# Optimization experiments

Measured on AMD Instinct MI355X. Metric: run time of the kernel, lower is better.

## Reference

```python
import jax, jax.numpy as jnp
import numpy as np

EMBED_DIM = 1024
NUM_HEADS = 16
HEAD_DIM = EMBED_DIM // NUM_HEADS
WINDOW = 3
N_RAND = 3
BLOCK = 64
BATCH = 2
SEQ = 2048


def _bigbird_mask(seq_len: int) -> np.ndarray:
    """Global + sliding-window + random block mask. True = attend.
    Deterministic (fixed numpy seed) stand-in for np.random.choice in the
    original; the mask is data-independent so it is a compile-time constant."""
    nb = -(-seq_len // BLOCK)  # ceil division
    mask = np.zeros((seq_len, seq_len), dtype=bool)
    g = min(BLOCK, seq_len)
    mask[:g, :] = True  # global rows
    mask[:, :g] = True  # global cols
    blk = np.arange(seq_len) // BLOCK
    # sliding window: block distance <= WINDOW (matches start/end block loop)
    mask |= np.abs(blk[:, None] - blk[None, :]) <= WINDOW
    rng = np.random.RandomState(0)
    for b in range(1, nb):
        avail = [x for x in range(1, nb) if abs(x - b) > WINDOW]
        if avail:
            sel = rng.choice(avail, size=min(N_RAND, len(avail)), replace=False)
            s0, s1 = b * BLOCK, min(seq_len, (b + 1) * BLOCK)
            for rb in sel:
                mask[s0:s1, rb * BLOCK:min(seq_len, (rb + 1) * BLOCK)] = True
    return mask


def setup_inputs() -> dict:
    key = jax.random.key(0)
    ks = jax.random.split(key, 9)
    E = EMBED_DIM
    std = E ** -0.5
    return {
        "hidden_states": jax.random.normal(ks[0], (BATCH, SEQ, E), jnp.float32),
        "wq": jax.random.normal(ks[1], (E, E), jnp.float32) * std,
        "bq": jnp.zeros((E,), jnp.float32),
        "wk": jax.random.normal(ks[2], (E, E), jnp.float32) * std,
        "bk": jnp.zeros((E,), jnp.float32),
        "wv": jax.random.normal(ks[3], (E, E), jnp.float32) * std,
        "bv": jnp.zeros((E,), jnp.float32),
        "wo": jax.random.normal(ks[4], (E, E), jnp.float32) * std,
        "bo": jnp.zeros((E,), jnp.float32),
    }


def reference(hidden_states, wq, bq, wk, bk, wv, bv, wo, bo):
    B, S, E = hidden_states.shape
    D = HEAD_DIM
    scale = D ** -0.5

    def proj(w, b):  # (B,S,E) -> (B,H,S,D)
        return (hidden_states @ w.T + b).reshape(B, S, NUM_HEADS, D).transpose(0, 2, 1, 3)

    q = proj(wq, bq)
    k = proj(wk, bk)
    v = proj(wv, bv)
    scores = jnp.einsum('bhqd,bhkd->bhqk', q, k) * scale  # dense, masked post-hoc (as in source)
    mask = jnp.asarray(_bigbird_mask(S))
    scores = jnp.where(mask[None, None, :, :], scores, -jnp.inf)
    attn = jax.nn.softmax(scores, axis=-1)
    out = jnp.einsum('bhqk,bhkd->bhqd', attn, v)
    out = out.transpose(0, 2, 1, 3).reshape(B, S, E)
    return out @ wo.T + bo
```

## Files before the change

### kernel.cpp

```cpp
#include <hip/hip_runtime.h>
#include <cstdint>
#include <math.h>


#define DEVI __device__ __forceinline__

typedef __bf16 bf16x8 __attribute__((ext_vector_type(8)));
typedef float floatx4 __attribute__((ext_vector_type(4)));
typedef unsigned short u16x8 __attribute__((ext_vector_type(8)));
typedef unsigned short u16x4 __attribute__((ext_vector_type(4)));
typedef unsigned short ushort_t;

typedef const __attribute__((address_space(1))) void* gptr_as1;
typedef __attribute__((address_space(3))) void* lptr_as3;

DEVI ushort_t f2bf(float f) {
  unsigned u = __float_as_uint(f);
  unsigned r = ((u >> 16) & 1u) + 0x7fffu;
  return (ushort_t)((u + r) >> 16);
}

DEVI void lds_load16(void* lds, const void* g) {
  __builtin_amdgcn_global_load_lds((gptr_as1)g, (lptr_as3)lds, 16, 0, 0);
}

DEVI floatx4 mfma16(bf16x8 a, bf16x8 b, floatx4 c) {
  return __builtin_amdgcn_mfma_f32_16x16x32_bf16(a, b, c, 0, 0, 0);
}

#define BARR() do { asm volatile("" ::: "memory"); \
                    __builtin_amdgcn_s_barrier();  \
                    asm volatile("" ::: "memory"); } while (0)
#define VMC(N) asm volatile("s_waitcnt vmcnt(" #N ")" ::: "memory")

struct MTState { unsigned mt[624]; int mti; };

constexpr unsigned mt_next(MTState& s) {
  if (s.mti >= 624) {
    for (int k = 0; k < 624; ++k) {
      unsigned y = (s.mt[k] & 0x80000000u) | (s.mt[(k + 1) % 624] & 0x7fffffffu);
      unsigned v = s.mt[(k + 397) % 624] ^ (y >> 1);
      if (y & 1u) v ^= 0x9908b0dfu;
      s.mt[k] = v;
    }
    s.mti = 0;
  }
  unsigned y = s.mt[s.mti++];
  y ^= y >> 11;
  y ^= (y << 7) & 0x9d2c5680u;
  y ^= (y << 15) & 0xefc60000u;
  y ^= y >> 18;
  return y;
}

constexpr unsigned mt_interval(MTState& s, unsigned mx) {
  if (mx == 0u) return 0u;
  unsigned msk = mx;
  msk |= msk >> 1; msk |= msk >> 2; msk |= msk >> 4; msk |= msk >> 8; msk |= msk >> 16;
  unsigned v = mt_next(s) & msk;
  while (v > mx) v = mt_next(s) & msk;
  return v;
}

struct MaskPack { unsigned char list[32][32]; int cnt[32]; };

constexpr MaskPack make_pack() {
  unsigned char m[32][32] = {};
  for (int i = 0; i < 32; ++i)
    for (int j = 0; j < 32; ++j) {
      int d = i - j; if (d < 0) d = -d;
      m[i][j] = (i == 0 || j == 0 || d <= 3) ? (unsigned char)1 : (unsigned char)0;
    }
  MTState st{};
  st.mt[0] = 0u;
  for (int i = 1; i < 624; ++i)
    st.mt[i] = 1812433253u * (st.mt[i - 1] ^ (st.mt[i - 1] >> 30)) + (unsigned)i;
  st.mti = 624;
  for (int b = 1; b < 32; ++b) {
    int avail[32] = {}; int n = 0;
    for (int x = 1; x < 32; ++x) {
      int d = x - b; if (d < 0) d = -d;
      if (d > 3) avail[n++] = x;
    }
    if (n == 0) continue;
    int perm[32] = {};
    for (int i = 0; i < n; ++i) perm[i] = i;
    for (int i = n - 1; i > 0; --i) {
      unsigned j = mt_interval(st, (unsigned)i);
      int t = perm[i]; perm[i] = perm[(int)j]; perm[(int)j] = t;
    }
    int take = n < 3 ? n : 3;
    for (int s = 0; s < take; ++s) m[b][avail[perm[s]]] = 1;
  }
  MaskPack P{};
  for (int i = 0; i < 32; ++i) {
    int c = 0;
    for (int j = 0; j < 32; ++j)
      if (m[i][j]) P.list[i][c++] = (unsigned char)j;
    P.cnt[i] = c;
  }
  return P;
}

__constant__ MaskPack MP = make_pack();

__global__ __launch_bounds__(256) void cvt_all(
    const float* __restrict__ hs, const float* __restrict__ wq,
    const float* __restrict__ wk, const float* __restrict__ wv,
    const float* __restrict__ wo,
    ushort_t* __restrict__ hs_bf, ushort_t* __restrict__ wq_bf,
    ushort_t* __restrict__ wk_bf, ushort_t* __restrict__ wv_bf,
    ushort_t* __restrict__ wo_bf) {
  const int i = blockIdx.x * 256 + threadIdx.x;
  const float* s;
  ushort_t* d;
  int j;
  if (i < 1048576) {
    s = hs; d = hs_bf; j = i;
  } else {
    const int t = (i - 1048576) >> 18;
    j = (i - 1048576) & 262143;
    s = t == 0 ? wq : (t == 1 ? wk : (t == 2 ? wv : wo));
    d = t == 0 ? wq_bf : (t == 1 ? wk_bf : (t == 2 ? wv_bf : wo_bf));
  }
  const float4 f = ((const float4*)s)[j];
  u16x4 o;
  o.x = f2bf(f.x); o.y = f2bf(f.y); o.z = f2bf(f.z); o.w = f2bf(f.w);
  ((u16x4*)d)[j] = o;
}

DEVI void stage_half(ushort_t* ldsb, const ushort_t* g, int w, int l) {
  lds_load16(ldsb + w * 1024 + l * 8, g);
  lds_load16(ldsb + w * 1024 + 512 + l * 8, g + 8192);
}

DEVI void rdA(bf16x8 (&a)[4][2], const ushort_t* base, int wm, int li, int quad) {
#pragma unroll
  for (int mi = 0; mi < 4; ++mi) {
    const int rh = wm * 64 + mi * 16 + li;
    const int sw = rh & 7;
#pragma unroll
    for (int ks = 0; ks < 2; ++ks)
      a[mi][ks] = *(const bf16x8*)(base + rh * 64 + (((ks * 4 + quad) ^ sw) << 3));
  }
}

DEVI void rdB(bf16x8 (&b)[2][2], const ushort_t* base, int wn, int li, int quad) {
#pragma unroll
  for (int ni = 0; ni < 2; ++ni) {
    const int rh = wn * 32 + ni * 16 + li;
    const int sw = rh & 7;
#pragma unroll
    for (int ks = 0; ks < 2; ++ks)
      b[ni][ks] = *(const bf16x8*)(base + rh * 64 + (((ks * 4 + quad) ^ sw) << 3));
  }
}

DEVI void mm16(floatx4 (&c)[4][2], const bf16x8 (&a)[4][2], const bf16x8 (&b)[2][2]) {
  __builtin_amdgcn_s_setprio(1);
#pragma unroll
  for (int ks = 0; ks < 2; ++ks)
#pragma unroll
    for (int mi = 0; mi < 4; ++mi)
#pragma unroll
      for (int ni = 0; ni < 2; ++ni)
        c[mi][ni] = mfma16(a[mi][ks], b[ni][ks], c[mi][ni]);
  __builtin_amdgcn_s_setprio(0);
}

__global__ __launch_bounds__(512, 2) void gemm_qkv_fused(
    const ushort_t* __restrict__ A,
    const ushort_t* __restrict__ W0, const ushort_t* __restrict__ W1,
    const ushort_t* __restrict__ W2,
    const float* __restrict__ bq, const float* __restrict__ bk,
    const float* __restrict__ bv,
    ushort_t* __restrict__ Qo, ushort_t* __restrict__ Ko,
    ushort_t* __restrict__ Vt) {
  __shared__ alignas(16) ushort_t LDS[2][2][2][8192];
  const int tid = threadIdx.x;
  const int w = tid >> 6, l = tid & 63, quad = l >> 4, li = l & 15;
  const int wm = w >> 2, wn = w & 3;
  const int bid = blockIdx.x;
  const int swz = (bid & 7) * 24 + (bid >> 3);
  const int m0 = (swz / 12) << 8;
  const int n0g = (swz % 12) << 8;
  const int z = n0g >> 10, n0l = n0g & 1023;
  const ushort_t* Bw = z == 0 ? W0 : (z == 1 ? W1 : W2);
  const float* bias = z == 0 ? bq : (z == 1 ? bk : bv);

  const int rst = w * 16 + (l >> 3);
  const int cst = ((l & 7) ^ (l >> 3)) << 3;
  const ushort_t* gA = A + (size_t)(m0 + rst) * 1024 + cst;
  const ushort_t* gB = Bw + (size_t)(n0l + rst) * 1024 + cst;

  const floatx4 fz = {0.0f, 0.0f, 0.0f, 0.0f};
  floatx4 acc[2][2][4][2];
#pragma unroll
  for (int qm = 0; qm < 2; ++qm)
#pragma unroll
    for (int qn = 0; qn < 2; ++qn)
#pragma unroll
      for (int mi = 0; mi < 4; ++mi)
#pragma unroll
        for (int ni = 0; ni < 2; ++ni) acc[qm][qn][mi][ni] = fz;

  bf16x8 a[4][2], b0[2][2], b1[2][2];

  stage_half(&LDS[0][0][0][0], gA, w, l);
  stage_half(&LDS[0][0][1][0], gA + 131072, w, l);
  stage_half(&LDS[0][1][0][0], gB, w, l);
  stage_half(&LDS[0][1][1][0], gB + 131072, w, l);
  stage_half(&LDS[1][0][0][0], gA + 64, w, l);
  stage_half(&LDS[1][1][0][0], gB + 64, w, l);
  stage_half(&LDS[1][1][1][0], gB + 131072 + 64, w, l);
  VMC(6);
  BARR();

#pragma unroll 1
  for (int it = 0; it < 8; ++it) {
    const bool pf = (it < 7);
    const int o_cy = (2 * it + 1) * 64;
    const int o_x = (2 * it + 2) * 64;
    const int o_y = (2 * it + 3) * 64;

    rdA(a, &LDS[0][0][0][0], wm, li, quad);
    rdB(b0, &LDS[0][1][0][0], wn, li, quad);
    stage_half(&LDS[1][0][1][0], gA + 131072 + o_cy, w, l);
    mm16(acc[0][0], a, b0);
    BARR();

    rdB(b1, &LDS[0][1][1][0], wn, li, quad);
    if (pf) stage_half(&LDS[0][0][0][0], gA + o_x, w, l);
    mm16(acc[0][1], a, b1);
    BARR();

    rdA(a, &LDS[0][0][1][0], wm, li, quad);
    if (pf) stage_half(&LDS[0][1][0][0], gB + o_x, w, l);
    mm16(acc[1][0], a, b0);
    BARR();

    if (pf) stage_half(&LDS[0][1][1][0], gB + 131072 + o_x, w, l);
    mm16(acc[1][1], a, b1);
    if (pf) { VMC(6); } else { VMC(0); }
    BARR();

    rdA(a, &LDS[1][0][0][0], wm, li, quad);
    rdB(b0, &LDS[1][1][0][0], wn, li, quad);
    if (pf) stage_half(&LDS[0][0][1][0], gA + 131072 + o_x, w, l);
    mm16(acc[0][0], a, b0);
    BARR();

    rdB(b1, &LDS[1][1][1][0], wn, li, quad);
    if (pf) stage_half(&LDS[1][0][0][0], gA + o_y, w, l);
    mm16(acc[0][1], a, b1);
    BARR();

    rdA(a, &LDS[1][0][1][0], wm, li, quad);
    if (pf) stage_half(&LDS[1][1][0][0], gB + o_y, w, l);
    mm16(acc[1][0], a, b0);
    BARR();

    if (pf) stage_half(&LDS[1][1][1][0], gB + 131072 + o_y, w, l);
    mm16(acc[1][1], a, b1);
    if (pf) { VMC(6); }
    BARR();
  }

  const float qs = (z == 0) ? 0.18033688011112042f : 1.0f;
#pragma unroll
  for (int Qm = 0; Qm < 2; ++Qm)
#pragma unroll
    for (int Qn = 0; Qn < 2; ++Qn)
#pragma unroll
      for (int ni = 0; ni < 2; ++ni) {
        const int col = n0l + Qn * 128 + wn * 32 + ni * 16 + li;
        const float bb_ = bias[col];
        if (z == 2) {
          const int hh = col >> 6, dd = col & 63;
#pragma unroll
          for (int mi = 0; mi < 4; ++mi) {
            const int row0 = m0 + Qm * 128 + wm * 64 + mi * 16 + quad * 4;
            const int bb = row0 >> 11, s0 = row0 & 2047;
            u16x4 pk;
#pragma unroll
            for (int r = 0; r < 4; ++r) pk[r] = f2bf(acc[Qm][Qn][mi][ni][r] + bb_);
            *(u16x4*)(Vt + (size_t)((bb * 16 + hh) * 64 + dd) * 2048 + s0) = pk;
          }
        } else {
          ushort_t* Co = (z == 0) ? Qo : Ko;
#pragma unroll
          for (int mi = 0; mi < 4; ++mi)
#pragma unroll
            for (int r = 0; r < 4; ++r) {
              const int row = m0 + Qm * 128 + wm * 64 + mi * 16 + quad * 4 + r;
              Co[(size_t)row * 1024 + col] = f2bf((acc[Qm][Qn][mi][ni][r] + bb_) * qs);
            }
        }
      }
}

__global__ __launch_bounds__(256) void gemm_o64(
    const ushort_t* __restrict__ A, const ushort_t* __restrict__ W,
    const float* __restrict__ bias, float* __restrict__ C) {
  constexpr int N = 1024, K = 1024;
  __shared__ alignas(16) ushort_t As[64 * 32];
  __shared__ alignas(16) ushort_t Bs[128 * 32];
  const int tid = threadIdx.x;
  const int w = tid >> 6, l = tid & 63, quad = l >> 4, li = l & 15;
  const int m0 = blockIdx.x * 64, n0 = blockIdx.y * 128;
  const int wm = (w >> 1) * 32, wn = (w & 1) * 64;

  const int lofA = w * 512 + l * 8;
  const int rA = lofA >> 5, cA = lofA & 31;
  const int lofB0 = (w * 2 + 0) * 512 + l * 8;
  const int lofB1 = (w * 2 + 1) * 512 + l * 8;
  const int rB0 = lofB0 >> 5, cB0 = lofB0 & 31;
  const int rB1 = lofB1 >> 5, cB1 = lofB1 & 31;
  const ushort_t* gA = A + (size_t)(m0 + rA) * K + cA;
  const ushort_t* gB0 = W + (size_t)(n0 + rB0) * K + cB0;
  const ushort_t* gB1 = W + (size_t)(n0 + rB1) * K + cB1;

  const floatx4 fzero = {0.0f, 0.0f, 0.0f, 0.0f};
  floatx4 acc[2][4];
#pragma unroll
  for (int i = 0; i < 2; ++i)
#pragma unroll
    for (int j = 0; j < 4; ++j) acc[i][j] = fzero;

  for (int k0 = 0; k0 < K; k0 += 32) {
    lds_load16(As + lofA, gA + k0);
    lds_load16(Bs + lofB0, gB0 + k0);
    lds_load16(Bs + lofB1, gB1 + k0);
    __syncthreads();
    bf16x8 af[2], bfr[4];
#pragma unroll
    for (int mi = 0; mi < 2; ++mi)
      af[mi] = *(const bf16x8*)(As + (wm + mi * 16 + li) * 32 + quad * 8);
#pragma unroll
    for (int ni = 0; ni < 4; ++ni)
      bfr[ni] = *(const bf16x8*)(Bs + (wn + ni * 16 + li) * 32 + quad * 8);
#pragma unroll
    for (int mi = 0; mi < 2; ++mi)
#pragma unroll
      for (int ni = 0; ni < 4; ++ni)
        acc[mi][ni] = mfma16(af[mi], bfr[ni], acc[mi][ni]);
    __syncthreads();
  }

#pragma unroll
  for (int ni = 0; ni < 4; ++ni) {
    const int col = n0 + wn + ni * 16 + li;
    const float bv = bias[col];
#pragma unroll
    for (int mi = 0; mi < 2; ++mi) {
#pragma unroll
      for (int r = 0; r < 4; ++r) {
        const int row = m0 + wm + mi * 16 + quad * 4 + r;
        C[(size_t)row * N + col] = acc[mi][ni][r] + bv;
      }
    }
  }
}

__global__ __launch_bounds__(256) void attn_kernel(
    const ushort_t* __restrict__ Q, const ushort_t* __restrict__ Kg,
    const ushort_t* __restrict__ Vtg, ushort_t* __restrict__ O,
    float* __restrict__ OP, float* __restrict__ LP) {
  __shared__ alignas(16) ushort_t Kls[64 * 72];
  __shared__ alignas(16) ushort_t Vls[64 * 72];
  __shared__ alignas(16) ushort_t Ps[4][16 * 76];

  const int tid = threadIdx.x;
  const int w = tid >> 6, l = tid & 63, quad = l >> 4, li = l & 15;
  const int hb = blockIdx.x;
  const int y = blockIdx.y;
  const bool partial = (y >= 31);
  const int qb = partial ? 0 : (y + 1);
  const int p = partial ? (y - 31) : 0;
  const int base = p * 11;
  const int nact = partial ? (32 - base < 11 ? 32 - base : 11) : MP.cnt[qb];

  const int h = hb & 15, b = hb >> 4;
  const size_t qoff = (size_t)b * 2048 * 1024 + (size_t)h * 64;
  const size_t vtoff = (size_t)hb * 64 * 2048;

  const int qrow = qb * 64 + w * 16 + li;
  const bf16x8 aq0 = *(const bf16x8*)(Q + qoff + (size_t)qrow * 1024 + quad * 8);
  const bf16x8 aq1 = *(const bf16x8*)(Q + qoff + (size_t)qrow * 1024 + 32 + quad * 8);

  const floatx4 fzero = {0.0f, 0.0f, 0.0f, 0.0f};
  floatx4 o_acc[4];
  float lp[4];
#pragma unroll
  for (int nt = 0; nt < 4; ++nt) o_acc[nt] = fzero;
#pragma unroll
  for (int r = 0; r < 4; ++r) lp[r] = 0.0f;

  const int r0 = w * 16 + (l >> 3);
  const int r1 = r0 + 8;
  const int cb = (l & 7) * 8;
  const ushort_t* kg0 = Kg + qoff + (size_t)r0 * 1024 + cb;
  const ushort_t* kg1 = Kg + qoff + (size_t)r1 * 1024 + cb;
  const ushort_t* vg0 = Vtg + vtoff + (size_t)r0 * 2048 + cb;
  const ushort_t* vg1 = Vtg + vtoff + (size_t)r1 * 2048 + cb;
  ushort_t* kd0 = Kls + r0 * 72 + cb;
  ushort_t* kd1 = Kls + r1 * 72 + cb;
  ushort_t* vd0 = Vls + r0 * 72 + cb;
  ushort_t* vd1 = Vls + r1 * 72 + cb;
  ushort_t* PsW = Ps[w];

  int kb = MP.list[qb][base];
  {
    const u16x8 a0 = *(const u16x8*)(kg0 + (size_t)kb * 65536);
    const u16x8 a1 = *(const u16x8*)(kg1 + (size_t)kb * 65536);
    const u16x8 b0 = *(const u16x8*)(vg0 + kb * 64);
    const u16x8 b1 = *(const u16x8*)(vg1 + kb * 64);
    *(u16x8*)kd0 = a0; *(u16x8*)kd1 = a1;
    *(u16x8*)vd0 = b0; *(u16x8*)vd1 = b1;
  }

  for (int i = 0; i < nact; ++i) {
    const bool pf = (i + 1 < nact);
    const int kbn = pf ? (int)MP.list[qb][base + i + 1] : 0;
    __syncthreads();

    u16x8 na0, na1, nb0, nb1;
    if (pf) {
      na0 = *(const u16x8*)(kg0 + (size_t)kbn * 65536);
      na1 = *(const u16x8*)(kg1 + (size_t)kbn * 65536);
      nb0 = *(const u16x8*)(vg0 + kbn * 64);
      nb1 = *(const u16x8*)(vg1 + kbn * 64);
    }

    floatx4 s[4];
#pragma unroll
    for (int nt = 0; nt < 4; ++nt) {
      const bf16x8 bk0 = *(const bf16x8*)(Kls + (nt * 16 + li) * 72 + quad * 8);
      const bf16x8 bk1 = *(const bf16x8*)(Kls + (nt * 16 + li) * 72 + 32 + quad * 8);
      s[nt] = mfma16(aq1, bk1, mfma16(aq0, bk0, fzero));
    }

#pragma unroll
    for (int nt = 0; nt < 4; ++nt)
#pragma unroll
      for (int r = 0; r < 4; ++r) {
        const float e = exp2f(s[nt][r]);
        lp[r] += e;
        PsW[(quad * 4 + r) * 76 + nt * 16 + li] = f2bf(e);
      }

#pragma unroll
    for (int c = 0; c < 2; ++c) {
      const bf16x8 pa = *(const bf16x8*)(PsW + li * 76 + c * 32 + quad * 8);
#pragma unroll
      for (int nt = 0; nt < 4; ++nt) {
        const bf16x8 vb = *(const bf16x8*)(Vls + (nt * 16 + li) * 72 + c * 32 + quad * 8);
        o_acc[nt] = mfma16(pa, vb, o_acc[nt]);
      }
    }

    __syncthreads();
    if (pf) {
      *(u16x8*)kd0 = na0; *(u16x8*)kd1 = na1;
      *(u16x8*)vd0 = nb0; *(u16x8*)vd1 = nb1;
    }
  }

#pragma unroll
  for (int stp = 1; stp <= 8; stp <<= 1)
#pragma unroll
    for (int r = 0; r < 4; ++r) lp[r] += __shfl_xor(lp[r], stp);

  if (!partial) {
#pragma unroll
    for (int r = 0; r < 4; ++r) {
      const float rinv = 1.0f / lp[r];
#pragma unroll
      for (int nt = 0; nt < 4; ++nt) {
        const float ov = o_acc[nt][r] * rinv;
        O[qoff + (size_t)(qb * 64 + w * 16 + quad * 4 + r) * 1024 + nt * 16 + li] = f2bf(ov);
      }
    }
  } else {
    float* O32 = OP + (size_t)(hb * 3 + p) * 4096;
    float* LPp = LP + (hb * 3 + p) * 64;
#pragma unroll
    for (int r = 0; r < 4; ++r) {
      const int row = w * 16 + quad * 4 + r;
#pragma unroll
      for (int nt = 0; nt < 4; ++nt)
        O32[row * 64 + nt * 16 + li] = o_acc[nt][r];
      if (li == 0) LPp[row] = lp[r];
    }
  }
}

__global__ __launch_bounds__(256) void combine_qb0(
    const float* __restrict__ OP, const float* __restrict__ LP,
    ushort_t* __restrict__ O) {
  const int hb = blockIdx.x;
  const int b = hb >> 4, h = hb & 15;
  const float* o0 = OP + (size_t)hb * 3 * 4096;
  const float* l0 = LP + hb * 3 * 64;
  for (int idx = threadIdx.x; idx < 4096; idx += 256) {
    const int q = idx >> 6, d = idx & 63;
    const float s = o0[idx] + o0[4096 + idx] + o0[8192 + idx];
    const float lsum = l0[q] + l0[64 + q] + l0[128 + q];
    O[(size_t)b * 2048 * 1024 + (size_t)q * 1024 + h * 64 + d] = f2bf(s / lsum);
  }
}

extern "C" void kernel_launch(void* const* d_in, const int* in_sizes, int n_in,
                              void* d_out, int out_size, void* d_ws, size_t ws_size,
                              hipStream_t stream) {
  const float* hs = (const float*)d_in[0];
  const float* wq = (const float*)d_in[1];
  const float* bq = (const float*)d_in[2];
  const float* wk = (const float*)d_in[3];
  const float* bk = (const float*)d_in[4];
  const float* wv = (const float*)d_in[5];
  const float* bv = (const float*)d_in[6];
  const float* wo = (const float*)d_in[7];
  const float* bo = (const float*)d_in[8];
  float* out = (float*)d_out;

  char* ws = (char*)d_ws;
  ushort_t* hs_bf = (ushort_t*)(ws);
  ushort_t* wq_bf = (ushort_t*)(ws + (8ull << 20));
  ushort_t* wk_bf = (ushort_t*)(ws + (10ull << 20));
  ushort_t* wv_bf = (ushort_t*)(ws + (12ull << 20));
  ushort_t* wo_bf = (ushort_t*)(ws + (14ull << 20));
  ushort_t* Qb = (ushort_t*)(ws + (16ull << 20));
  ushort_t* Kb = (ushort_t*)(ws + (24ull << 20));
  ushort_t* Vt = (ushort_t*)(ws + (32ull << 20));
  ushort_t* AO = hs_bf;
  float* OP = (float*)(ws + (10ull << 20));
  float* LP = (float*)((char*)OP + 32 * 3 * 4096 * sizeof(float));

  cvt_all<<<8192, 256, 0, stream>>>(hs, wq, wk, wv, wo,
                                    hs_bf, wq_bf, wk_bf, wv_bf, wo_bf);

  gemm_qkv_fused<<<192, 512, 0, stream>>>(hs_bf, wq_bf, wk_bf, wv_bf,
                                          bq, bk, bv, Qb, Kb, Vt);

  dim3 ga(32, 34, 1);
  attn_kernel<<<ga, 256, 0, stream>>>(Qb, Kb, Vt, AO, OP, LP);

  combine_qb0<<<32, 256, 0, stream>>>(OP, LP, AO);

  dim3 go(64, 8, 1);
  gemm_o64<<<go, 256, 0, stream>>>(AO, wo_bf, bo, out);
}
```

Measured before the change: 191.2 us.

## Process KV blocks in pairs with double-buffered K/V and P aliased into K LDS

```diff
diff --git a/kernel.cpp b/kernel.cpp
--- a/kernel.cpp
+++ b/kernel.cpp
@@ -366,9 +366,8 @@
     const ushort_t* __restrict__ Q, const ushort_t* __restrict__ Kg,
     const ushort_t* __restrict__ Vtg, ushort_t* __restrict__ O,
     float* __restrict__ OP, float* __restrict__ LP) {
-  __shared__ alignas(16) ushort_t Kls[64 * 72];
-  __shared__ alignas(16) ushort_t Vls[64 * 72];
-  __shared__ alignas(16) ushort_t Ps[4][16 * 76];
+  __shared__ alignas(16) ushort_t Kls[2][4608];
+  __shared__ alignas(16) ushort_t Vls[2][4608];
 
   const int tid = threadIdx.x;
   const int w = tid >> 6, l = tid & 63, quad = l >> 4, li = l & 15;
@@ -403,66 +402,139 @@
   const ushort_t* kg1 = Kg + qoff + (size_t)r1 * 1024 + cb;
   const ushort_t* vg0 = Vtg + vtoff + (size_t)r0 * 2048 + cb;
   const ushort_t* vg1 = Vtg + vtoff + (size_t)r1 * 2048 + cb;
-  ushort_t* kd0 = Kls + r0 * 72 + cb;
-  ushort_t* kd1 = Kls + r1 * 72 + cb;
-  ushort_t* vd0 = Vls + r0 * 72 + cb;
-  ushort_t* vd1 = Vls + r1 * 72 + cb;
-  ushort_t* PsW = Ps[w];
-
-  int kb = MP.list[qb][base];
+  const int sd0 = r0 * 72 + cb;
+  const int sd1 = r1 * 72 + cb;
+
+  ushort_t* Pall = &Kls[0][0];
+  ushort_t* PA = Pall + w * 1088;
+  ushort_t* PB = Pall + 4352 + w * 1088;
+
   {
-    const u16x8 a0 = *(const u16x8*)(kg0 + (size_t)kb * 65536);
-    const u16x8 a1 = *(const u16x8*)(kg1 + (size_t)kb * 65536);
-    const u16x8 b0 = *(const u16x8*)(vg0 + kb * 64);
-    const u16x8 b1 = *(const u16x8*)(vg1 + kb * 64);
-    *(u16x8*)kd0 = a0; *(u16x8*)kd1 = a1;
-    *(u16x8*)vd0 = b0; *(u16x8*)vd1 = b1;
-  }
-
-  for (int i = 0; i < nact; ++i) {
-    const bool pf = (i + 1 < nact);
-    const int kbn = pf ? (int)MP.list[qb][base + i + 1] : 0;
+    const int kb0 = MP.list[qb][base];
+    const u16x8 a0 = *(const u16x8*)(kg0 + (size_t)kb0 * 65536);
+    const u16x8 a1 = *(const u16x8*)(kg1 + (size_t)kb0 * 65536);
+    const u16x8 b0 = *(const u16x8*)(vg0 + kb0 * 64);
+    const u16x8 b1 = *(const u16x8*)(vg1 + kb0 * 64);
+    *(u16x8*)(&Kls[0][0] + sd0) = a0; *(u16x8*)(&Kls[0][0] + sd1) = a1;
+    *(u16x8*)(&Vls[0][0] + sd0) = b0; *(u16x8*)(&Vls[0][0] + sd1) = b1;
+    if (nact > 1) {
+      const int kb1 = MP.list[qb][base + 1];
+      const u16x8 c0 = *(const u16x8*)(kg0 + (size_t)kb1 * 65536);
+      const u16x8 c1 = *(const u16x8*)(kg1 + (size_t)kb1 * 65536);
+      const u16x8 d0 = *(const u16x8*)(vg0 + kb1 * 64);
+      const u16x8 d1 = *(const u16x8*)(vg1 + kb1 * 64);
+      *(u16x8*)(&Kls[1][0] + sd0) = c0; *(u16x8*)(&Kls[1][0] + sd1) = c1;
+      *(u16x8*)(&Vls[1][0] + sd0) = d0; *(u16x8*)(&Vls[1][0] + sd1) = d1;
+    }
+  }
+  __syncthreads();
+
+  const int npair = nact >> 1;
+#pragma unroll 1
+  for (int ip = 0; ip < npair; ++ip) {
+    const int i0 = 2 * ip;
+    const bool pfA = (i0 + 2 < nact);
+    const bool pfB = (i0 + 3 < nact);
+
+    u16x8 nkA0, nkA1, nvA0, nvA1, nkB0, nkB1, nvB0, nvB1;
+    if (pfA) {
+      const int kbn = MP.list[qb][base + i0 + 2];
+      nkA0 = *(const u16x8*)(kg0 + (size_t)kbn * 65536);
+      nkA1 = *(const u16x8*)(kg1 + (size_t)kbn * 65536);
+      nvA0 = *(const u16x8*)(vg0 + kbn * 64);
+      nvA1 = *(const u16x8*)(vg1 + kbn * 64);
+    }
+    if (pfB) {
+      const int kbn = MP.list[qb][base + i0 + 3];
+      nkB0 = *(const u16x8*)(kg0 + (size_t)kbn * 65536);
+      nkB1 = *(const u16x8*)(kg1 + (size_t)kbn * 65536);
+      nvB0 = *(const u16x8*)(vg0 + kbn * 64);
+      nvB1 = *(const u16x8*)(vg1 + kbn * 64);
+    }
+
+    floatx4 sA[4], sB[4];
+#pragma unroll
+    for (int nt = 0; nt < 4; ++nt) {
+      const bf16x8 k0 = *(const bf16x8*)(&Kls[0][0] + (nt * 16 + li) * 72 + quad * 8);
+      const bf16x8 k1 = *(const bf16x8*)(&Kls[0][0] + (nt * 16 + li) * 72 + 32 + quad * 8);
+      sA[nt] = mfma16(aq1, k1, mfma16(aq0, k0, fzero));
+    }
+#pragma unroll
+    for (int nt = 0; nt < 4; ++nt) {
+      const bf16x8 k0 = *(const bf16x8*)(&Kls[1][0] + (nt * 16 + li) * 72 + quad * 8);
+      const bf16x8 k1 = *(const bf16x8*)(&Kls[1][0] + (nt * 16 + li) * 72 + 32 + quad * 8);
+      sB[nt] = mfma16(aq1, k1, mfma16(aq0, k0, fzero));
+    }
     __syncthreads();
 
-    u16x8 na0, na1, nb0, nb1;
-    if (pf) {
-      na0 = *(const u16x8*)(kg0 + (size_t)kbn * 65536);
-      na1 = *(const u16x8*)(kg1 + (size_t)kbn * 65536);
-      nb0 = *(const u16x8*)(vg0 + kbn * 64);
-      nb1 = *(const u16x8*)(vg1 + kbn * 64);
-    }
-
-    floatx4 s[4];
+#pragma unroll
+    for (int nt = 0; nt < 4; ++nt)
+#pragma unroll
+      for (int r = 0; r < 4; ++r) {
+        const float eA = exp2f(sA[nt][r]);
+        lp[r] += eA;
+        PA[(quad * 4 + r) * 68 + nt * 16 + li] = f2bf(eA);
+        const float eB = exp2f(sB[nt][r]);
+        lp[r] += eB;
+        PB[(quad * 4 + r) * 68 + nt * 16 + li] = f2bf(eB);
+      }
+
+#pragma unroll
+    for (int c = 0; c < 2; ++c) {
+      const bf16x8 pa = *(const bf16x8*)(PA + li * 68 + c * 32 + quad * 8);
+#pragma unroll
+      for (int nt = 0; nt < 4; ++nt) {
+        const bf16x8 vb = *(const bf16x8*)(&Vls[0][0] + (nt * 16 + li) * 72 + c * 32 + quad * 8);
+        o_acc[nt] = mfma16(pa, vb, o_acc[nt]);
+      }
+    }
+#pragma unroll
+    for (int c = 0; c < 2; ++c) {
+      const bf16x8 pa = *(const bf16x8*)(PB + li * 68 + c * 32 + quad * 8);
+#pragma unroll
+      for (int nt = 0; nt < 4; ++nt) {
+        const bf16x8 vb = *(const bf16x8*)(&Vls[1][0] + (nt * 16 + li) * 72 + c * 32 + quad * 8);
+        o_acc[nt] = mfma16(pa, vb, o_acc[nt]);
+      }
+    }
+    __syncthreads();
+
+    if (pfA) {
+      *(u16x8*)(&Kls[0][0] + sd0) = nkA0; *(u16x8*)(&Kls[0][0] + sd1) = nkA1;
+      *(u16x8*)(&Vls[0][0] + sd0) = nvA0; *(u16x8*)(&Vls[0][0] + sd1) = nvA1;
+    }
+    if (pfB) {
+      *(u16x8*)(&Kls[1][0] + sd0) = nkB0; *(u16x8*)(&Kls[1][0] + sd1) = nkB1;
+      *(u16x8*)(&Vls[1][0] + sd0) = nvB0; *(u16x8*)(&Vls[1][0] + sd1) = nvB1;
+    }
+    if (pfA) __syncthreads();
+  }
+
+  if (nact & 1) {
+    floatx4 sA[4];
 #pragma unroll
     for (int nt = 0; nt < 4; ++nt) {
-      const bf16x8 bk0 = *(const bf16x8*)(Kls + (nt * 16 + li) * 72 + quad * 8);
-      const bf16x8 bk1 = *(const bf16x8*)(Kls + (nt * 16 + li) * 72 + 32 + quad * 8);
-      s[nt] = mfma16(aq1, bk1, mfma16(aq0, bk0, fzero));
-    }
-
+      const bf16x8 k0 = *(const bf16x8*)(&Kls[0][0] + (nt * 16 + li) * 72 + quad * 8);
+      const bf16x8 k1 = *(const bf16x8*)(&Kls[0][0] + (nt * 16 + li) * 72 + 32 + quad * 8);
+      sA[nt] = mfma16(aq1, k1, mfma16(aq0, k0, fzero));
+    }
+    __syncthreads();
 #pragma unroll
     for (int nt = 0; nt < 4; ++nt)
 #pragma unroll
       for (int r = 0; r < 4; ++r) {
-        const float e = exp2f(s[nt][r]);
+        const float e = exp2f(sA[nt][r]);
         lp[r] += e;
-        PsW[(quad * 4 + r) * 76 + nt * 16 + li] = f2bf(e);
-      }
-
+        PA[(quad * 4 + r) * 68 + nt * 16 + li] = f2bf(e);
+      }
 #pragma unroll
     for (int c = 0; c < 2; ++c) {
-      const bf16x8 pa = *(const bf16x8*)(PsW + li * 76 + c * 32 + quad * 8);
+      const bf16x8 pa = *(const bf16x8*)(PA + li * 68 + c * 32 + quad * 8);
 #pragma unroll
       for (int nt = 0; nt < 4; ++nt) {
-        const bf16x8 vb = *(const bf16x8*)(Vls + (nt * 16 + li) * 72 + c * 32 + quad * 8);
+        const bf16x8 vb = *(const bf16x8*)(&Vls[0][0] + (nt * 16 + li) * 72 + c * 32 + quad * 8);
         o_acc[nt] = mfma16(pa, vb, o_acc[nt]);
       }
-    }
-
-    __syncthreads();
-    if (pf) {
-      *(u16x8*)kd0 = na0; *(u16x8*)kd1 = na1;
-      *(u16x8*)vd0 = nb0; *(u16x8*)vd1 = nb1;
     }
   }
 
```

Measured after the change: 197.1 us. +3.1%, slower.
